# Kernel optimization log

Measured on AMD Instinct MI355X. Metric: run time of the kernel, lower is better.

Reference implementation:

```python
import jax, jax.numpy as jnp
import numpy as np

HIDDEN = 128
N_NODES = 50000
N_EDGES = 640000


def setup_inputs() -> dict:
    key = jax.random.key(0)
    k1, k2, k3, k4, k5, k6, k7 = jax.random.split(key, 7)
    z = jax.random.normal(k1, (N_NODES, HIDDEN), dtype=jnp.float32)
    edge_index = jax.random.randint(k2, (2, N_EDGES), 0, N_NODES, dtype=jnp.int64)
    # Linear params (torch default uniform(-1/sqrt(fan_in), 1/sqrt(fan_in)))
    b1 = 1.0 / np.sqrt(2 * HIDDEN)
    W1 = jax.random.uniform(k3, (HIDDEN, 2 * HIDDEN), jnp.float32, -b1, b1)
    bias1 = jax.random.uniform(k4, (HIDDEN,), jnp.float32, -b1, b1)
    b2 = 1.0 / np.sqrt(HIDDEN)
    W2 = jax.random.uniform(k5, (1, HIDDEN), jnp.float32, -b2, b2)
    bias2 = jax.random.uniform(k6, (1,), jnp.float32, -b2, b2)
    return {"z": z, "W1": W1, "bias1": bias1, "W2": W2, "bias2": bias2,
            "edge_index": edge_index}


def reference(z, W1, bias1, W2, bias2, edge_index):
    # Gather endpoint embeddings: [E, H] each
    z_src = z[edge_index[0]]
    z_dst = z[edge_index[1]]
    h = jnp.concatenate([z_src, z_dst], axis=-1)  # [E, 2H]
    h = jax.nn.relu(h @ W1.T + bias1)             # [E, H]
    out = h @ W2.T + bias2                        # [E, 1]
    return out.reshape(-1)
```

## Files before the change

### kernel.cpp

```cpp
#include <hip/hip_runtime.h>
#include <hip/hip_bf16.h>


#define N_NODES 50000
#define N_EDGES 640000
#define H 128

using bf16 = __hip_bfloat16;
typedef __attribute__((ext_vector_type(8))) short short8;
typedef __attribute__((ext_vector_type(4))) float f32x4;

static __device__ __forceinline__ short bfbits(float x) {
  __hip_bfloat16 h = __float2bfloat16(x);
  return *reinterpret_cast<short*>(&h);
}

static __device__ __forceinline__ short8 pack8(float4 a, float4 b) {
  short8 r;
  r[0] = bfbits(a.x); r[1] = bfbits(a.y); r[2] = bfbits(a.z); r[3] = bfbits(a.w);
  r[4] = bfbits(b.x); r[5] = bfbits(b.y); r[6] = bfbits(b.z); r[7] = bfbits(b.w);
  return r;
}

#define ZUNITS (N_NODES * H / 8)
#define WUNITS (2 * H * H / 8)

__global__ __launch_bounds__(256) void to_bf16(
    const float* __restrict__ z, const float* __restrict__ W1,
    bf16* __restrict__ zb, bf16* __restrict__ Wb) {
  const int u = blockIdx.x * 256 + threadIdx.x;
  const float4* src;
  bf16* dst;
  if (u < ZUNITS) {
    src = reinterpret_cast<const float4*>(z) + (size_t)u * 2;
    dst = zb + (size_t)u * 8;
  } else if (u < ZUNITS + WUNITS) {
    const int w = u - ZUNITS;
    const int o = w >> 4;
    const int k8 = (w & 15) * 8;
    src = reinterpret_cast<const float4*>(W1 + (size_t)(o & (H - 1)) * (2 * H) +
                                          (o >> 7) * H + k8);
    dst = Wb + (size_t)o * H + k8;
  } else {
    return;
  }
  *reinterpret_cast<short8*>(dst) = pack8(src[0], src[1]);
}

__global__ __launch_bounds__(256) void precompute_uv(
    const bf16* __restrict__ zb, const bf16* __restrict__ Wb,
    bf16* __restrict__ U, bf16* __restrict__ V) {
  __shared__ bf16 tile[32][2 * H + 8];
  const int lane = threadIdx.x & 63;
  const int s = threadIdx.x >> 6;
  const int l15 = lane & 15, quad = lane >> 4;
  const int nodebase = blockIdx.x * 32;

  short8 wf[4][4];
#pragma unroll
  for (int t = 0; t < 4; ++t) {
    const int o = s * 64 + t * 16 + l15;
    const bf16* wp = Wb + (size_t)o * H + quad * 8;
#pragma unroll
    for (int q = 0; q < 4; ++q)
      wf[t][q] = *reinterpret_cast<const short8*>(wp + q * 32);
  }
  int node[2];
  short8 zf[2][4];
#pragma unroll
  for (int m = 0; m < 2; ++m) {
    node[m] = nodebase + m * 16 + l15;
    const int nodeC = node[m] < N_NODES ? node[m] : N_NODES - 1;
    const bf16* zp = zb + (size_t)nodeC * H + quad * 8;
#pragma unroll
    for (int q = 0; q < 4; ++q)
      zf[m][q] = *reinterpret_cast<const short8*>(zp + q * 32);
  }

  f32x4 acc[2][4] = {};
#pragma unroll
  for (int m = 0; m < 2; ++m)
#pragma unroll
    for (int t = 0; t < 4; ++t)
#pragma unroll
      for (int q = 0; q < 4; ++q)
        acc[m][t] =
            __builtin_amdgcn_mfma_f32_16x16x32_bf16(wf[t][q], zf[m][q], acc[m][t], 0, 0, 0);

#pragma unroll
  for (int m = 0; m < 2; ++m) {
    const int nl = m * 16 + l15;
#pragma unroll
    for (int t = 0; t < 4; ++t) {
      const int o = s * 64 + t * 16 + quad * 4;
      ushort4 st;
      st.x = (unsigned short)bfbits(acc[m][t][0]);
      st.y = (unsigned short)bfbits(acc[m][t][1]);
      st.z = (unsigned short)bfbits(acc[m][t][2]);
      st.w = (unsigned short)bfbits(acc[m][t][3]);
      *reinterpret_cast<ushort4*>(&tile[nl][o]) = st;
    }
  }
  __syncthreads();

#pragma unroll
  for (int half = 0; half < 2; ++half) {
    bf16* base = half ? V : U;
#pragma unroll
    for (int it = 0; it < 2; ++it) {
      const int nl = s * 8 + it * 4 + (lane >> 4);
      const int oc = (lane & 15) * 8;
      const short8 v = *reinterpret_cast<const short8*>(&tile[nl][half * H + oc]);
      const int n = nodebase + nl;
      if (n < N_NODES)
        *reinterpret_cast<short8*>(base + (size_t)n * H + oc) = v;
    }
  }
}

static __device__ __forceinline__ void acc2(unsigned u, unsigned v,
                                            float b1lo, float b1hi,
                                            float w2lo, float w2hi, float& sum) {
  const float ulo = __uint_as_float(u << 16);
  const float uhi = __uint_as_float(u & 0xffff0000u);
  const float vlo = __uint_as_float(v << 16);
  const float vhi = __uint_as_float(v & 0xffff0000u);
  float h0 = ulo + vlo + b1lo; h0 = fmaxf(h0, 0.f);
  float h1 = uhi + vhi + b1hi; h1 = fmaxf(h1, 0.f);
  sum = fmaf(h0, w2lo, sum);
  sum = fmaf(h1, w2hi, sum);
}

__global__ __launch_bounds__(256, 4) void edge_decode(
    const int* __restrict__ eidx, const bf16* __restrict__ Ub,
    const bf16* __restrict__ Vb, const float* __restrict__ bias1,
    const float* __restrict__ W2, const float* __restrict__ bias2,
    float* __restrict__ out) {
  const int lane = threadIdx.x & 63;
  const int w = blockIdx.x * 4 + (int)(threadIdx.x >> 6);
  const int chunk = w * 64;
  const int e8 = lane & 7;

  float b1r[16], w2r[16];
  const float4* bp = reinterpret_cast<const float4*>(bias1 + e8 * 16);
  const float4* wp = reinterpret_cast<const float4*>(W2 + e8 * 16);
#pragma unroll
  for (int q = 0; q < 4; ++q) {
    const float4 b = bp[q], wv = wp[q];
    b1r[q * 4 + 0] = b.x; b1r[q * 4 + 1] = b.y; b1r[q * 4 + 2] = b.z; b1r[q * 4 + 3] = b.w;
    w2r[q * 4 + 0] = wv.x; w2r[q * 4 + 1] = wv.y; w2r[q * 4 + 2] = wv.z; w2r[q * 4 + 3] = wv.w;
  }
  const float b2 = bias2[0];

  const int src = eidx[chunk + lane];
  const int dst = eidx[N_EDGES + chunk + lane];
  const uint4* U4 = reinterpret_cast<const uint4*>(Ub);
  const uint4* V4 = reinterpret_cast<const uint4*>(Vb);

  float res = 0.f;
#pragma unroll
  for (int half = 0; half < 2; ++half) {
    uint4 ua[4], ub[4], va[4], vb[4];
#pragma unroll
    for (int j = 0; j < 4; ++j) {
      const int i = half * 4 + j;
      const int sl = (lane & 56) + i;
      const int s_i = __shfl(src, sl);
      const int d_i = __shfl(dst, sl);
      const uint4* up = U4 + (size_t)s_i * 16 + e8 * 2;
      const uint4* vp = V4 + (size_t)d_i * 16 + e8 * 2;
      ua[j] = up[0]; ub[j] = up[1];
      va[j] = vp[0]; vb[j] = vp[1];
    }
#pragma unroll
    for (int j = 0; j < 4; ++j) {
      const int i = half * 4 + j;
      float sum = 0.f;
      acc2(ua[j].x, va[j].x, b1r[0],  b1r[1],  w2r[0],  w2r[1],  sum);
      acc2(ua[j].y, va[j].y, b1r[2],  b1r[3],  w2r[2],  w2r[3],  sum);
      acc2(ua[j].z, va[j].z, b1r[4],  b1r[5],  w2r[4],  w2r[5],  sum);
      acc2(ua[j].w, va[j].w, b1r[6],  b1r[7],  w2r[6],  w2r[7],  sum);
      acc2(ub[j].x, vb[j].x, b1r[8],  b1r[9],  w2r[8],  w2r[9],  sum);
      acc2(ub[j].y, vb[j].y, b1r[10], b1r[11], w2r[10], w2r[11], sum);
      acc2(ub[j].z, vb[j].z, b1r[12], b1r[13], w2r[12], w2r[13], sum);
      acc2(ub[j].w, vb[j].w, b1r[14], b1r[15], w2r[14], w2r[15], sum);
      sum += __shfl_xor(sum, 1);
      sum += __shfl_xor(sum, 2);
      sum += __shfl_xor(sum, 4);
      if (e8 == i) res = sum + b2;
    }
  }
  out[chunk + lane] = res;
}

extern "C" void kernel_launch(void* const* d_in, const int* in_sizes, int n_in,
                              void* d_out, int out_size, void* d_ws, size_t ws_size,
                              hipStream_t stream) {
  const float* z     = (const float*)d_in[0];
  const float* W1    = (const float*)d_in[1];
  const float* bias1 = (const float*)d_in[2];
  const float* W2    = (const float*)d_in[3];
  const float* bias2 = (const float*)d_in[4];
  const int*   eidx  = (const int*)d_in[5];
  float* out = (float*)d_out;

  bf16* U  = (bf16*)d_ws;
  bf16* V  = U + (size_t)N_NODES * H;
  bf16* zb = V + (size_t)N_NODES * H;
  bf16* Wb = zb + (size_t)N_NODES * H;

  hipLaunchKernelGGL(to_bf16, dim3((ZUNITS + WUNITS) / 256), dim3(256), 0, stream,
                     z, W1, zb, Wb);
  hipLaunchKernelGGL(precompute_uv, dim3((N_NODES + 31) / 32), dim3(256), 0, stream,
                     zb, Wb, U, V);
  hipLaunchKernelGGL(edge_decode, dim3(N_EDGES / 64 / 4), dim3(256), 0, stream,
                     eidx, U, V, bias1, W2, bias2, out);
}
```

Baseline: 143.1 us.

## Fuse z fp32-to-bf16 conversion into node projection kernel via LDS loads

```diff
diff --git a/kernel.cpp b/kernel.cpp
--- a/kernel.cpp
+++ b/kernel.cpp
@@ -9,6 +9,11 @@
 using bf16 = __hip_bfloat16;
 typedef __attribute__((ext_vector_type(8))) short short8;
 typedef __attribute__((ext_vector_type(4))) float f32x4;
+
+#define GLD_LDS16(g, l)                                                     \
+  __builtin_amdgcn_global_load_lds(                                         \
+      (const __attribute__((address_space(1))) void*)(g),                   \
+      (__attribute__((address_space(3))) void*)(l), 16, 0, 0)
 
 static __device__ __forceinline__ short bfbits(float x) {
   __hip_bfloat16 h = __float2bfloat16(x);
@@ -22,60 +27,64 @@
   return r;
 }
 
-#define ZUNITS (N_NODES * H / 8)
-#define WUNITS (2 * H * H / 8)
-
-__global__ __launch_bounds__(256) void to_bf16(
-    const float* __restrict__ z, const float* __restrict__ W1,
-    bf16* __restrict__ zb, bf16* __restrict__ Wb) {
+__global__ __launch_bounds__(256) void w_to_bf16(const float* __restrict__ W1,
+                                                 bf16* __restrict__ Wb) {
   const int u = blockIdx.x * 256 + threadIdx.x;
-  const float4* src;
-  bf16* dst;
-  if (u < ZUNITS) {
-    src = reinterpret_cast<const float4*>(z) + (size_t)u * 2;
-    dst = zb + (size_t)u * 8;
-  } else if (u < ZUNITS + WUNITS) {
-    const int w = u - ZUNITS;
-    const int o = w >> 4;
-    const int k8 = (w & 15) * 8;
-    src = reinterpret_cast<const float4*>(W1 + (size_t)(o & (H - 1)) * (2 * H) +
-                                          (o >> 7) * H + k8);
-    dst = Wb + (size_t)o * H + k8;
-  } else {
-    return;
-  }
-  *reinterpret_cast<short8*>(dst) = pack8(src[0], src[1]);
-}
+  const int o = u >> 4, k8 = (u & 15) * 8;
+  const float4* src = reinterpret_cast<const float4*>(
+      W1 + (size_t)(o & (H - 1)) * (2 * H) + (o >> 7) * H + k8);
+  *reinterpret_cast<short8*>(Wb + (size_t)o * H + k8) = pack8(src[0], src[1]);
+}
+
+#define HP 136
 
 __global__ __launch_bounds__(256) void precompute_uv(
-    const bf16* __restrict__ zb, const bf16* __restrict__ Wb,
+    const float* __restrict__ z, const bf16* __restrict__ Wb,
     bf16* __restrict__ U, bf16* __restrict__ V) {
-  __shared__ bf16 tile[32][2 * H + 8];
-  const int lane = threadIdx.x & 63;
-  const int s = threadIdx.x >> 6;
+  __shared__ float ldsF[32 * H];
+  __shared__ bf16 ldsH[32 * HP];
+  const int tid = threadIdx.x;
+  const int lane = tid & 63;
+  const int s = tid >> 6;
   const int l15 = lane & 15, quad = lane >> 4;
   const int nodebase = blockIdx.x * 32;
 
+  {
+    int r0 = nodebase + s * 8;
+    if (r0 > N_NODES - 8) r0 = N_NODES - 8;
+    const float* gsrc = z + (size_t)r0 * H + lane * 4;
+    float* ldst = ldsF + s * 8 * H;
+#pragma unroll
+    for (int j = 0; j < 4; ++j) GLD_LDS16(gsrc + j * 256, ldst + j * 256);
+  }
+
   short8 wf[4][4];
 #pragma unroll
   for (int t = 0; t < 4; ++t) {
-    const int o = s * 64 + t * 16 + l15;
-    const bf16* wp = Wb + (size_t)o * H + quad * 8;
+    const bf16* wp = Wb + (size_t)(s * 64 + t * 16 + l15) * H + quad * 8;
 #pragma unroll
     for (int q = 0; q < 4; ++q)
       wf[t][q] = *reinterpret_cast<const short8*>(wp + q * 32);
   }
-  int node[2];
+
+  __syncthreads();
+
+  {
+    const int row = tid >> 3, off = (tid & 7) * 16;
+    const float4* fp = reinterpret_cast<const float4*>(ldsF + row * H + off);
+    const float4 a = fp[0], b = fp[1], c = fp[2], d = fp[3];
+    *reinterpret_cast<short8*>(&ldsH[row * HP + off]) = pack8(a, b);
+    *reinterpret_cast<short8*>(&ldsH[row * HP + off + 8]) = pack8(c, d);
+  }
+  __syncthreads();
+
   short8 zf[2][4];
 #pragma unroll
-  for (int m = 0; m < 2; ++m) {
-    node[m] = nodebase + m * 16 + l15;
-    const int nodeC = node[m] < N_NODES ? node[m] : N_NODES - 1;
-    const bf16* zp = zb + (size_t)nodeC * H + quad * 8;
+  for (int m = 0; m < 2; ++m)
 #pragma unroll
     for (int q = 0; q < 4; ++q)
-      zf[m][q] = *reinterpret_cast<const short8*>(zp + q * 32);
-  }
+      zf[m][q] = *reinterpret_cast<const short8*>(
+          &ldsH[(m * 16 + l15) * HP + quad * 8 + q * 32]);
 
   f32x4 acc[2][4] = {};
 #pragma unroll
@@ -87,6 +96,7 @@
         acc[m][t] =
             __builtin_amdgcn_mfma_f32_16x16x32_bf16(wf[t][q], zf[m][q], acc[m][t], 0, 0, 0);
 
+  bf16* epi = reinterpret_cast<bf16*>(ldsF);
 #pragma unroll
   for (int m = 0; m < 2; ++m) {
     const int nl = m * 16 + l15;
@@ -98,7 +108,7 @@
       st.y = (unsigned short)bfbits(acc[m][t][1]);
       st.z = (unsigned short)bfbits(acc[m][t][2]);
       st.w = (unsigned short)bfbits(acc[m][t][3]);
-      *reinterpret_cast<ushort4*>(&tile[nl][o]) = st;
+      *reinterpret_cast<ushort4*>(epi + nl * 256 + o) = st;
     }
   }
   __syncthreads();
@@ -110,7 +120,7 @@
     for (int it = 0; it < 2; ++it) {
       const int nl = s * 8 + it * 4 + (lane >> 4);
       const int oc = (lane & 15) * 8;
-      const short8 v = *reinterpret_cast<const short8*>(&tile[nl][half * H + oc]);
+      const short8 v = *reinterpret_cast<const short8*>(epi + nl * 256 + half * H + oc);
       const int n = nodebase + nl;
       if (n < N_NODES)
         *reinterpret_cast<short8*>(base + (size_t)n * H + oc) = v;
@@ -206,13 +216,11 @@
 
   bf16* U  = (bf16*)d_ws;
   bf16* V  = U + (size_t)N_NODES * H;
-  bf16* zb = V + (size_t)N_NODES * H;
-  bf16* Wb = zb + (size_t)N_NODES * H;
-
-  hipLaunchKernelGGL(to_bf16, dim3((ZUNITS + WUNITS) / 256), dim3(256), 0, stream,
-                     z, W1, zb, Wb);
+  bf16* Wb = V + (size_t)N_NODES * H;
+
+  hipLaunchKernelGGL(w_to_bf16, dim3(16), dim3(256), 0, stream, W1, Wb);
   hipLaunchKernelGGL(precompute_uv, dim3((N_NODES + 31) / 32), dim3(256), 0, stream,
-                     zb, Wb, U, V);
+                     z, Wb, U, V);
   hipLaunchKernelGGL(edge_decode, dim3(N_EDGES / 64 / 4), dim3(256), 0, stream,
                      eidx, U, V, bias1, W2, bias2, out);
 }
```

Result: faster. 137.2 us (-4.1%).
